# Optimization experiments

Hardware: AMD Instinct MI355X
Metric: run time of the kernel (lower is better)

Reference implementation:

```python
import jax, jax.numpy as jnp
import numpy as np

TOP_K = 2          # routed top_k = top_k - num_shared_experts = 3 - 1
CAP_FACTOR = 1.1   # capacity_factor


def setup_inputs() -> dict:
    key = jax.random.key(0)
    ks = jax.random.split(key, 12)
    B, S, D, E = 4, 2048, 1024, 7
    s = 0.02
    return {
        "x": jax.random.normal(ks[0], (B, S, D), jnp.float32),
        "noise": jax.random.normal(ks[1], (B, S, E), jnp.float32),
        "Wr": jax.random.normal(ks[2], (D, E)) * s, "br": jnp.zeros((E,)),
        "Wn": jax.random.normal(ks[3], (D, E)) * s, "bn": jnp.zeros((E,)),
        "W1": jax.random.normal(ks[4], (E, D, D)) * s, "b1": jnp.zeros((E, D)),
        "W2": jax.random.normal(ks[5], (E, D, D)) * s, "b2": jnp.zeros((E, D)),
        "Ws1": jax.random.normal(ks[6], (D, D)) * s, "bs1": jnp.zeros((D,)),
        "Ws2": jax.random.normal(ks[7], (D, D)) * s, "bs2": jnp.zeros((D,)),
    }


def reference(x, noise, Wr, br, Wn, bn, W1, b1, W2, b2, Ws1, bs1, Ws2, bs2):
    B, S, D = x.shape
    E = Wr.shape[1]
    N = B * S
    C = int(N * TOP_K / E * CAP_FACTOR)  # per-expert capacity (static)

    # shared expert (Dropout inactive at inference)
    x_shared = jax.nn.relu(x @ Ws1 + bs1) @ Ws2 + bs2

    # --- noisy top-k router ---
    logits = x @ Wr + br
    noisy = logits + noise * jax.nn.softplus(x @ Wn + bn)
    vals, idx = jax.lax.top_k(noisy, TOP_K)                    # [B,S,K]
    onehot = jax.nn.one_hot(idx, E, dtype=x.dtype)             # [B,S,K,E]
    probs_k = jax.nn.softmax(vals, axis=-1)                    # softmax over -inf-masked logits == softmax over top-k vals
    router_probs = jnp.einsum('bske,bsk->bse', onehot, probs_k)
    expert_mask = onehot.sum(-2)
    lbl = E * (router_probs.mean((0, 1)) * expert_mask.mean((0, 1))).sum()

    # --- capacity-limited dispatch, first-come-first-served in flat token order ---
    flat_x = x.reshape(N, D)
    flat_g = router_probs.reshape(N, E)
    m = (expert_mask.reshape(N, E) > 0).T                      # [E,N] token->expert assignment
    pos = jnp.cumsum(m.astype(jnp.int32), axis=1) - 1          # slot within expert
    valid = m & (pos < C)
    token = jnp.arange(N, dtype=jnp.int32)
    dest = jnp.where(valid, jnp.arange(E, dtype=jnp.int32)[:, None] * C + pos, E * C)
    idxs = jnp.full((E * C + 1,), N, dtype=jnp.int32)
    idxs = idxs.at[dest.reshape(-1)].set(jnp.broadcast_to(token, (E, N)).reshape(-1))
    idxs = idxs[:E * C].reshape(E, C)                          # token id per slot, N = padding

    xpad = jnp.concatenate([flat_x, jnp.zeros((1, D), x.dtype)], axis=0)
    gpad = jnp.concatenate([flat_g, jnp.zeros((1, E), x.dtype)], axis=0)
    xe = xpad[idxs]                                            # [E,C,D]
    h = jax.nn.relu(jnp.einsum('ecd,edh->ech', xe, W1) + b1[:, None, :])
    out = jnp.einsum('ech,ehd->ecd', h, W2) + b2[:, None, :]
    g = (gpad[idxs] * jnp.eye(E, dtype=x.dtype)[:, None, :]).sum(-1)  # [E,C] gate per slot
    slot_valid = (idxs < N).astype(x.dtype)
    weighted = out * (g * slot_valid)[..., None]

    upd = jnp.zeros((N + 1, D), x.dtype).at[idxs.reshape(-1)].add(weighted.reshape(-1, D))[:N]
    final = upd.reshape(B, S, D) + x_shared
    return final, lbl
```

## Files before the change

kernel.cpp:

```cpp
#include <hip/hip_runtime.h>
#include <math.h>

typedef unsigned short u16;
typedef __attribute__((ext_vector_type(4))) float f32x4;
typedef __bf16 bf16x8 __attribute__((ext_vector_type(8)));

#define NTOK 8192
#define DDIM 1024
#define NEXP 7
#define CAPC 2574
#define CPAD 2688
#define EBLK 1176
#define TBLK 1688

__device__ inline float bf2f(u16 u) {
    union { unsigned int i; float f; } c; c.i = ((unsigned int)u) << 16; return c.f;
}
__device__ inline u16 f2bf(float f) {
    union { float f; unsigned int i; } c; c.f = f;
    unsigned int u = c.i;
    unsigned int r = (u + 0x7fffu + ((u >> 16) & 1u)) >> 16;
    return (u16)r;
}

__device__ inline void gl2lds16(const u16* g, const u16* l) {
    __builtin_amdgcn_global_load_lds(
        (const __attribute__((address_space(1))) unsigned int*)g,
        (__attribute__((address_space(3))) unsigned int*)l, 16, 0, 0);
}

__global__ void k_zero(float* out, long n) {
    long i = (long)blockIdx.x * 256 + threadIdx.x;
    long stride = (long)gridDim.x * 256;
    for (; i < n; i += stride) out[i] = 0.f;
}

__global__ void k_prep(const float* __restrict__ x, u16* __restrict__ xb,
                       int* __restrict__ slot_token, u16* __restrict__ zrow,
                       const float* __restrict__ W1, const float* __restrict__ Ws1,
                       u16* __restrict__ Wt, u16* __restrict__ Wst,
                       const float* __restrict__ W2, const float* __restrict__ Ws2,
                       u16* __restrict__ Wt2, u16* __restrict__ Wst2) {
    int bid = blockIdx.x, tid = threadIdx.x;
    if (bid < 4096) {
        int gid = bid * 256 + tid;
        int i = gid * 8;
        float4 a = *(const float4*)(x + i);
        float4 b = *(const float4*)(x + i + 4);
        ushort4 o0; o0.x = f2bf(a.x); o0.y = f2bf(a.y); o0.z = f2bf(a.z); o0.w = f2bf(a.w);
        ushort4 o1; o1.x = f2bf(b.x); o1.y = f2bf(b.y); o1.z = f2bf(b.z); o1.w = f2bf(b.w);
        *(ushort4*)(xb + i) = o0;
        *(ushort4*)(xb + i + 4) = o1;
        if (gid < DDIM) zrow[gid] = 0;
        if (gid < NEXP * CPAD) slot_token[gid] = NTOK;
        return;
    }
    int phase2 = (bid >= 8192);
    int tb = bid - (phase2 ? 8192 : 4096);
    const float* srcE = phase2 ? W2 : W1;
    const float* srcS = phase2 ? Ws2 : Ws1;
    u16* dE = phase2 ? Wt2 : Wt;
    u16* dS = phase2 ? Wst2 : Wst;
    int z = tb >> 9; int rem = tb & 511;
    int y = rem >> 2; int xq = rem & 3;
    const float* src; u16* dst;
    if (z < 7) { src = srcE + (long)z * 1048576; dst = dE + (long)z * 1048576; }
    else       { src = srcS;                     dst = dS; }
    int n = xq * 256 + tid;
    int k0 = y * 8;
    u16 v[8];
#pragma unroll
    for (int j = 0; j < 8; ++j) v[j] = f2bf(src[(long)(k0 + j) * 1024 + n]);
    ushort4 a; a.x = v[0]; a.y = v[1]; a.z = v[2]; a.w = v[3];
    ushort4 b; b.x = v[4]; b.y = v[5]; b.z = v[6]; b.w = v[7];
    *(ushort4*)(dst + (long)n * 1024 + k0) = a;
    *(ushort4*)(dst + (long)n * 1024 + k0 + 4) = b;
}

__global__ void k_transpose(const float* __restrict__ srcE, const float* __restrict__ srcS,
                            u16* __restrict__ Wt, u16* __restrict__ Wst) {
    int z = blockIdx.z;
    const float* src; u16* dst;
    if (z < 7) { src = srcE + (long)z * 1048576; dst = Wt + (long)z * 1048576; }
    else       { src = srcS;                     dst = Wst; }
    int n = blockIdx.x * 256 + threadIdx.x;
    int k0 = blockIdx.y * 8;
    u16 v[8];
#pragma unroll
    for (int j = 0; j < 8; ++j) v[j] = f2bf(src[(long)(k0 + j) * 1024 + n]);
    ushort4 a; a.x = v[0]; a.y = v[1]; a.z = v[2]; a.w = v[3];
    ushort4 b; b.x = v[4]; b.y = v[5]; b.z = v[6]; b.w = v[7];
    *(ushort4*)(dst + (long)n * 1024 + k0) = a;
    *(ushort4*)(dst + (long)n * 1024 + k0 + 4) = b;
}

__global__ __launch_bounds__(512) void k_router(
    const float* __restrict__ x,
    const float* __restrict__ Wr, const float* __restrict__ Wn,
    double* __restrict__ arO, double* __restrict__ anO) {
    __shared__ float swr[7168];
    __shared__ float swn[7168];
    int tid = threadIdx.x;
    for (int i = tid; i < 7168; i += 512) { swr[i] = Wr[i]; swn[i] = Wn[i]; }
    __syncthreads();
    int lane = tid & 63, wv = tid >> 6;
    int t = blockIdx.x * 8 + wv;
    double ar[7] = {0,0,0,0,0,0,0}, an[7] = {0,0,0,0,0,0,0};
    for (int j = 0; j < 16; ++j) {
        int d = j * 64 + lane;
        double xd = (double)x[t * 1024 + d];
#pragma unroll
        for (int e = 0; e < 7; ++e) {
            ar[e] += xd * (double)swr[d * 7 + e];
            an[e] += xd * (double)swn[d * 7 + e];
        }
    }
#pragma unroll
    for (int e = 0; e < 7; ++e) {
        for (int o = 32; o > 0; o >>= 1) {
            ar[e] += __shfl_xor(ar[e], o);
            an[e] += __shfl_xor(an[e], o);
        }
    }
    if (lane == 0) {
#pragma unroll
        for (int e = 0; e < 7; ++e) { arO[t * 7 + e] = ar[e]; anO[t * 7 + e] = an[e]; }
    }
}

__global__ void k_tail(const double* __restrict__ arO, const double* __restrict__ anO,
                       const float* __restrict__ noise,
                       const float* __restrict__ br, const float* __restrict__ bn,
                       int* __restrict__ idx0, int* __restrict__ idx1,
                       float* __restrict__ p0, float* __restrict__ p1,
                       int* __restrict__ cntA, double* __restrict__ sumA) {
    int t = blockIdx.x * 256 + threadIdx.x;
    int lane = threadIdx.x & 63;
    double best = -1e300, second = -1e300; int b0 = 0, b1 = 0;
#pragma unroll
    for (int e = 0; e < 7; ++e) {
        double lg = arO[t * 7 + e] + (double)br[e];
        double z  = anO[t * 7 + e] + (double)bn[e];
        double sp = (z > 30.0) ? (z + log1p(exp(-z))) : log1p(exp(z));
        double v  = lg + (double)noise[t * 7 + e] * sp;
        if (v > best)        { second = best; b1 = b0; best = v; b0 = e; }
        else if (v > second) { second = v; b1 = e; }
    }
    double ex = exp(second - best);
    float q0 = (float)(1.0 / (1.0 + ex));
    float q1 = (float)(ex / (1.0 + ex));
    idx0[t] = b0; idx1[t] = b1; p0[t] = q0; p1[t] = q1;
    int chunk = t >> 6;
    double dq0 = (double)q0, dq1 = (double)q1;
#pragma unroll
    for (int e = 0; e < 7; ++e) {
        unsigned long long m = __ballot((b0 == e) || (b1 == e));
        double q = (b0 == e ? dq0 : 0.0) + (b1 == e ? dq1 : 0.0);
        for (int o = 32; o > 0; o >>= 1) q += __shfl_xor(q, o);
        if (lane == 0) { cntA[e * 128 + chunk] = __popcll(m); sumA[e * 128 + chunk] = q; }
    }
}

__global__ void k_scanbase(const int* __restrict__ cntA, const double* __restrict__ sumA,
                           int* __restrict__ baseA, int* __restrict__ cnt,
                           float* __restrict__ out) {
    __shared__ int s[128];
    __shared__ double rd[128];
    __shared__ int rawc[7];
    __shared__ double ps[7];
    int tid = threadIdx.x;
    for (int e = 0; e < 7; ++e) {
        int v = 0;
        if (tid < 128) { v = cntA[e * 128 + tid]; s[tid] = v; }
        if (tid < 128) rd[tid] = sumA[e * 128 + tid];
        __syncthreads();
        for (int o = 1; o < 128; o <<= 1) {
            int add = 0;
            if (tid < 128 && tid >= o) add = s[tid - o];
            __syncthreads();
            if (tid < 128) s[tid] += add;
            __syncthreads();
        }
        if (tid < 128) baseA[e * 128 + tid] = s[tid] - v;
        if (tid == 127) { rawc[e] = s[127]; cnt[e] = (s[127] < CAPC) ? s[127] : CAPC; }
        for (int o = 64; o > 0; o >>= 1) {
            if (tid < o) rd[tid] += rd[tid + o];
            __syncthreads();
        }
        if (tid == 0) ps[e] = rd[0];
        __syncthreads();
    }
    if (tid == 0) {
        double acc = 0.0;
        for (int e = 0; e < 7; ++e) acc += ps[e] * (double)rawc[e];
        out[(long)NTOK * DDIM] = (float)(7.0 * acc / (8192.0 * 8192.0));
    }
}

__global__ void k_assign(const int* __restrict__ idx0, const int* __restrict__ idx1,
                         const int* __restrict__ baseA, int* __restrict__ slot_token,
                         int* __restrict__ ts0, int* __restrict__ ts1) {
    int lane = threadIdx.x & 63;
    int chunk = (blockIdx.x * 256 + threadIdx.x) >> 6;
    int t = chunk * 64 + lane;
    int i0 = idx0[t], i1 = idx1[t];
    int myts0 = -1, myts1 = -1;
    unsigned long long lt = (1ull << lane) - 1ull;
#pragma unroll
    for (int e = 0; e < 7; ++e) {
        bool has = (i0 == e) || (i1 == e);
        unsigned long long m = __ballot(has);
        int pre = __popcll(m & lt);
        int pos = baseA[e * 128 + chunk] + pre;
        if (has && pos < CAPC) {
            int slot = e * CPAD + pos;
            slot_token[slot] = t;
            if (i0 == e) myts0 = slot; else myts1 = slot;
        }
    }
    ts0[t] = myts0; ts1[t] = myts1;
}

template <bool GATHER, bool MODE_H>
__global__ __launch_bounds__(256) void k_gemm(
    const u16* __restrict__ AbaseE, const u16* __restrict__ AbaseS,
    const int* __restrict__ gidx, const u16* __restrict__ zrow,
    const u16* __restrict__ WtE, const u16* __restrict__ WtS,
    const float* __restrict__ biasE, const float* __restrict__ biasS,
    u16* __restrict__ outE, u16* __restrict__ outS,
    const int* __restrict__ cnt) {
    __shared__ __align__(16) u16 ldsA[128 * 64];
    __shared__ __align__(16) u16 ldsB[128 * 64];
    int bid = blockIdx.x;
    int tid = threadIdx.x, lane = tid & 63, wv = tid >> 6;
    int lrow = lane >> 3, lkg = lane & 7;
    int kgs = lkg ^ lrow;

    int e = 0, my, nx;
    const u16* Ab; const u16* Bb; const float* bias; u16* outp;
    bool gather = false;
    if (bid < EBLK) {
        e = bid / 168; int r = bid % 168; my = r >> 3; nx = r & 7;
        if (my * 128 >= cnt[e]) return;
        Ab = AbaseE + (GATHER ? 0L : (long)e * CPAD * 1024);
        Bb = WtE + ((long)e << 20);
        bias = biasE + e * 1024;
        outp = outE + (long)e * CPAD * 1024;
        gather = GATHER;
    } else {
        int sb = bid - EBLK; my = sb >> 3; nx = sb & 7;
        Ab = AbaseS; Bb = WtS; bias = biasS; outp = outS;
    }
    int m0 = my * 128, n0 = nx * 128;

    const u16* arow[4];
    const u16* brow[4];
#pragma unroll
    for (int i = 0; i < 4; ++i) {
        int r = (wv * 4 + i) * 8 + lrow;
        if (gather) {
            int tok = gidx[e * CPAD + m0 + r];
            arow[i] = (tok < NTOK) ? (AbaseE + (long)tok * DDIM) : zrow;
        } else {
            arow[i] = Ab + (long)(m0 + r) * DDIM;
        }
        brow[i] = Bb + (long)(n0 + r) * DDIM;
    }
    f32x4 acc[4][4];
#pragma unroll
    for (int a = 0; a < 4; ++a)
#pragma unroll
        for (int b = 0; b < 4; ++b) { f32x4 z = {0.f, 0.f, 0.f, 0.f}; acc[a][b] = z; }

    int wm = (wv >> 1) * 64, wn = (wv & 1) * 64;
    int rl = lane & 15, quad = lane >> 4;

    for (int k0 = 0; k0 < 1024; k0 += 64) {
#pragma unroll
        for (int i = 0; i < 4; ++i) {
            gl2lds16(arow[i] + k0 + kgs * 8, &ldsA[(wv * 4 + i) * 512]);
            gl2lds16(brow[i] + k0 + kgs * 8, &ldsB[(wv * 4 + i) * 512]);
        }
        __syncthreads();
#pragma unroll
        for (int ks = 0; ks < 2; ++ks) {
            int kg = ks * 4 + quad;
            bf16x8 af[4], bf[4];
#pragma unroll
            for (int mi = 0; mi < 4; ++mi) {
                int row = wm + mi * 16 + rl;
                af[mi] = *(const bf16x8*)&ldsA[row * 64 + (kg ^ (row & 7)) * 8];
            }
#pragma unroll
            for (int ni = 0; ni < 4; ++ni) {
                int row = wn + ni * 16 + rl;
                bf[ni] = *(const bf16x8*)&ldsB[row * 64 + (kg ^ (row & 7)) * 8];
            }
#pragma unroll
            for (int mi = 0; mi < 4; ++mi)
#pragma unroll
                for (int ni = 0; ni < 4; ++ni)
                    acc[mi][ni] = __builtin_amdgcn_mfma_f32_16x16x32_bf16(
                        af[mi], bf[ni], acc[mi][ni], 0, 0, 0);
        }
        __syncthreads();
    }
#pragma unroll
    for (int ni = 0; ni < 4; ++ni) {
        int col = n0 + wn + ni * 16 + rl;
        float bv = bias[col];
#pragma unroll
        for (int mi = 0; mi < 4; ++mi) {
            int rowb = m0 + wm + mi * 16 + quad * 4;
#pragma unroll
            for (int r = 0; r < 4; ++r) {
                float v = acc[mi][ni][r] + bv;
                if constexpr (MODE_H) v = v > 0.f ? v : 0.f;
                outp[(long)(rowb + r) * DDIM + col] = f2bf(v);
            }
        }
    }
}

__global__ __launch_bounds__(256) void k_combine(
    const u16* __restrict__ Xs, const u16* __restrict__ OutE,
    const int* __restrict__ ts0, const int* __restrict__ ts1,
    const float* __restrict__ p0, const float* __restrict__ p1,
    float* __restrict__ out) {
    int b = blockIdx.x;
    int d = threadIdx.x * 4;
    long base = (long)b * DDIM + d;
    ushort4 xs4 = *(const ushort4*)(Xs + base);
    float r0 = bf2f(xs4.x), r1 = bf2f(xs4.y), r2 = bf2f(xs4.z), r3 = bf2f(xs4.w);
    int s0 = ts0[b], s1 = ts1[b];
    if (s0 >= 0) {
        float g = p0[b];
        ushort4 o4 = *(const ushort4*)(OutE + (long)s0 * DDIM + d);
        r0 += g * bf2f(o4.x); r1 += g * bf2f(o4.y); r2 += g * bf2f(o4.z); r3 += g * bf2f(o4.w);
    }
    if (s1 >= 0) {
        float g = p1[b];
        ushort4 o4 = *(const ushort4*)(OutE + (long)s1 * DDIM + d);
        r0 += g * bf2f(o4.x); r1 += g * bf2f(o4.y); r2 += g * bf2f(o4.z); r3 += g * bf2f(o4.w);
    }
    float4 w; w.x = r0; w.y = r1; w.z = r2; w.w = r3;
    *(float4*)(out + base) = w;
}

extern "C" void kernel_launch(void* const* d_in, const int* in_sizes, int n_in,
                              void* d_out, int out_size, void* d_ws, size_t ws_size,
                              hipStream_t stream) {
    const float* x    = (const float*)d_in[0];
    const float* noise= (const float*)d_in[1];
    const float* Wr   = (const float*)d_in[2];
    const float* br   = (const float*)d_in[3];
    const float* Wn   = (const float*)d_in[4];
    const float* bn   = (const float*)d_in[5];
    const float* W1   = (const float*)d_in[6];
    const float* b1   = (const float*)d_in[7];
    const float* W2   = (const float*)d_in[8];
    const float* b2   = (const float*)d_in[9];
    const float* Ws1  = (const float*)d_in[10];
    const float* bs1  = (const float*)d_in[11];
    const float* Ws2  = (const float*)d_in[12];
    const float* bs2  = (const float*)d_in[13];
    float* out = (float*)d_out;
    char* ws = (char*)d_ws;

    size_t off = 0;
    auto alloc = [&](size_t bytes) { size_t o = off; off += (bytes + 255) & ~(size_t)255; return o; };
    u16*  Wt   = (u16*)(ws + alloc(7ull * 1048576 * 2));
    u16*  Wst  = (u16*)(ws + alloc(1048576ull * 2));
    u16*  xb   = (u16*)(ws + alloc((size_t)NTOK * 1024 * 2));
    u16*  He   = (u16*)(ws + alloc((size_t)NEXP * CPAD * 1024 * 2));
    u16*  Hs   = (u16*)(ws + alloc((size_t)NTOK * 1024 * 2));
    u16*  OutE = (u16*)(ws + alloc((size_t)NEXP * CPAD * 1024 * 2));
    u16*  Xs   = (u16*)(ws + alloc((size_t)NTOK * 1024 * 2));
    int*  idx0 = (int*)(ws + alloc(NTOK * 4));
    int*  idx1 = (int*)(ws + alloc(NTOK * 4));
    float* p0  = (float*)(ws + alloc(NTOK * 4));
    float* p1  = (float*)(ws + alloc(NTOK * 4));
    int*  ts0  = (int*)(ws + alloc(NTOK * 4));
    int*  ts1  = (int*)(ws + alloc(NTOK * 4));
    int*  slot_token = (int*)(ws + alloc(NEXP * CPAD * 4));
    int*  cntA = (int*)(ws + alloc(7 * 128 * 4));
    int*  baseA= (int*)(ws + alloc(7 * 128 * 4));
    double* sumA = (double*)(ws + alloc(7 * 128 * 8));
    int*  cnt    = (int*)(ws + alloc(8 * 4));
    u16*  zrow   = (u16*)(ws + alloc(1024 * 2));
    double* arO  = (double*)(ws + alloc((size_t)NTOK * 7 * 8));
    double* anO  = (double*)(ws + alloc((size_t)NTOK * 7 * 8));
    size_t base_off = off;
    u16*  Wt2  = (u16*)(ws + alloc(7ull * 1048576 * 2));
    u16*  Wst2 = (u16*)(ws + alloc(1048576ull * 2));

    if (base_off > ws_size) {
        k_zero<<<2048, 256, 0, stream>>>(out, (long)out_size);
        return;
    }
    bool sep = (off <= ws_size);
    if (!sep) { Wt2 = Wt; Wst2 = Wst; }

    k_prep<<<sep ? 12288 : 8192, 256, 0, stream>>>(
        x, xb, slot_token, zrow, W1, Ws1, Wt, Wst, W2, Ws2, Wt2, Wst2);
    k_router<<<1024, 512, 0, stream>>>(x, Wr, Wn, arO, anO);
    k_tail<<<32, 256, 0, stream>>>(arO, anO, noise, br, bn, idx0, idx1, p0, p1, cntA, sumA);
    k_scanbase<<<1, 256, 0, stream>>>(cntA, sumA, baseA, cnt, out);
    k_assign<<<32, 256, 0, stream>>>(idx0, idx1, baseA, slot_token, ts0, ts1);

    k_gemm<true, true><<<TBLK, 256, 0, stream>>>(
        xb, xb, slot_token, zrow, Wt, Wst, b1, bs1, He, Hs, cnt);

    if (!sep)
        k_transpose<<<dim3(4, 128, 8), 256, 0, stream>>>(W2, Ws2, Wt, Wst);

    k_gemm<false, false><<<TBLK, 256, 0, stream>>>(
        He, Hs, nullptr, zrow, Wt2, Wst2, b2, bs2, OutE, Xs, cnt);

    k_combine<<<NTOK, 256, 0, stream>>>(Xs, OutE, ts0, ts1, p0, p1, out);
    (void)in_sizes; (void)n_in; (void)out_size;
}
```

Measured before the change: 401.1 us.

## Double-buffer GEMM LDS with inline-asm reads, tile weight transpose via LDS, parallelize scan

```diff
diff --git a/kernel.cpp b/kernel.cpp
--- a/kernel.cpp
+++ b/kernel.cpp
@@ -3,6 +3,7 @@
 
 typedef unsigned short u16;
 typedef __attribute__((ext_vector_type(4))) float f32x4;
+typedef __attribute__((ext_vector_type(4))) int v4i;
 typedef __bf16 bf16x8 __attribute__((ext_vector_type(8)));
 
 #define NTOK 8192
@@ -29,10 +30,45 @@
         (__attribute__((address_space(3))) unsigned int*)l, 16, 0, 0);
 }
 
+#define SCHED0()  __builtin_amdgcn_sched_barrier(0)
+#define PRIO1()   __builtin_amdgcn_s_setprio(1)
+#define PRIO0()   __builtin_amdgcn_s_setprio(0)
+#define LGKM8()   asm volatile("s_waitcnt lgkmcnt(8)")
+#define LGKM0()   asm volatile("s_waitcnt lgkmcnt(0)")
+
 __global__ void k_zero(float* out, long n) {
     long i = (long)blockIdx.x * 256 + threadIdx.x;
     long stride = (long)gridDim.x * 256;
     for (; i < n; i += stride) out[i] = 0.f;
+}
+
+__device__ inline void tile_transpose(const float* __restrict__ src, u16* __restrict__ dst,
+                                      int k0, int n0, int tid, u16 (*tbuf)[256]) {
+#pragma unroll
+    for (int p = 0; p < 16; ++p) {
+        int kl = p * 16 + (tid >> 4);
+        int nl = (tid & 15) * 4;
+        float4 v = *(const float4*)(src + (long)(k0 + kl) * 1024 + n0 + nl);
+        int s = (tid & 7) << 3;
+        int kx = kl ^ s;
+        tbuf[nl + 0][kx] = f2bf(v.x);
+        tbuf[nl + 1][kx] = f2bf(v.y);
+        tbuf[nl + 2][kx] = f2bf(v.z);
+        tbuf[nl + 3][kx] = f2bf(v.w);
+    }
+    __syncthreads();
+#pragma unroll
+    for (int q = 0; q < 8; ++q) {
+        int nl = q * 8 + (tid >> 5);
+        int kl = (tid & 31) * 8;
+        int s = ((nl >> 2) & 7) << 3;
+        const u16* pr = &tbuf[nl][kl ^ s];
+        ushort4 a = *(const ushort4*)pr;
+        ushort4 b = *(const ushort4*)(pr + 4);
+        u16* pd = dst + (long)(n0 + nl) * 1024 + k0 + kl;
+        *(ushort4*)pd = a;
+        *(ushort4*)(pd + 4) = b;
+    }
 }
 
 __global__ void k_prep(const float* __restrict__ x, u16* __restrict__ xb,
@@ -41,6 +77,7 @@
                        u16* __restrict__ Wt, u16* __restrict__ Wst,
                        const float* __restrict__ W2, const float* __restrict__ Ws2,
                        u16* __restrict__ Wt2, u16* __restrict__ Wst2) {
+    __shared__ u16 tbuf[64][256];
     int bid = blockIdx.x, tid = threadIdx.x;
     if (bid < 4096) {
         int gid = bid * 256 + tid;
@@ -55,43 +92,35 @@
         if (gid < NEXP * CPAD) slot_token[gid] = NTOK;
         return;
     }
-    int phase2 = (bid >= 8192);
-    int tb = bid - (phase2 ? 8192 : 4096);
-    const float* srcE = phase2 ? W2 : W1;
-    const float* srcS = phase2 ? Ws2 : Ws1;
-    u16* dE = phase2 ? Wt2 : Wt;
-    u16* dS = phase2 ? Wst2 : Wst;
-    int z = tb >> 9; int rem = tb & 511;
-    int y = rem >> 2; int xq = rem & 3;
+    int tb = bid - 4096;
+    int set = tb >> 9;
+    int t9 = tb & 511;
+    int z = t9 >> 6;
+    int rem = t9 & 63;
+    int k0 = (rem >> 4) * 256;
+    int n0 = (rem & 15) * 64;
+    const float* srcE = set ? W2 : W1;
+    const float* srcS = set ? Ws2 : Ws1;
+    u16* dE = set ? Wt2 : Wt;
+    u16* dS = set ? Wst2 : Wst;
     const float* src; u16* dst;
     if (z < 7) { src = srcE + (long)z * 1048576; dst = dE + (long)z * 1048576; }
     else       { src = srcS;                     dst = dS; }
-    int n = xq * 256 + tid;
-    int k0 = y * 8;
-    u16 v[8];
-#pragma unroll
-    for (int j = 0; j < 8; ++j) v[j] = f2bf(src[(long)(k0 + j) * 1024 + n]);
-    ushort4 a; a.x = v[0]; a.y = v[1]; a.z = v[2]; a.w = v[3];
-    ushort4 b; b.x = v[4]; b.y = v[5]; b.z = v[6]; b.w = v[7];
-    *(ushort4*)(dst + (long)n * 1024 + k0) = a;
-    *(ushort4*)(dst + (long)n * 1024 + k0 + 4) = b;
+    tile_transpose(src, dst, k0, n0, tid, tbuf);
 }
 
 __global__ void k_transpose(const float* __restrict__ srcE, const float* __restrict__ srcS,
                             u16* __restrict__ Wt, u16* __restrict__ Wst) {
-    int z = blockIdx.z;
+    __shared__ u16 tbuf[64][256];
+    int bid = blockIdx.x, tid = threadIdx.x;
+    int z = bid >> 6;
+    int rem = bid & 63;
+    int k0 = (rem >> 4) * 256;
+    int n0 = (rem & 15) * 64;
     const float* src; u16* dst;
     if (z < 7) { src = srcE + (long)z * 1048576; dst = Wt + (long)z * 1048576; }
     else       { src = srcS;                     dst = Wst; }
-    int n = blockIdx.x * 256 + threadIdx.x;
-    int k0 = blockIdx.y * 8;
-    u16 v[8];
-#pragma unroll
-    for (int j = 0; j < 8; ++j) v[j] = f2bf(src[(long)(k0 + j) * 1024 + n]);
-    ushort4 a; a.x = v[0]; a.y = v[1]; a.z = v[2]; a.w = v[3];
-    ushort4 b; b.x = v[4]; b.y = v[5]; b.z = v[6]; b.w = v[7];
-    *(ushort4*)(dst + (long)n * 1024 + k0) = a;
-    *(ushort4*)(dst + (long)n * 1024 + k0 + 4) = b;
+    tile_transpose(src, dst, k0, n0, tid, tbuf);
 }
 
 __global__ __launch_bounds__(512) void k_router(
@@ -164,35 +193,33 @@
 __global__ void k_scanbase(const int* __restrict__ cntA, const double* __restrict__ sumA,
                            int* __restrict__ baseA, int* __restrict__ cnt,
                            float* __restrict__ out) {
-    __shared__ int s[128];
-    __shared__ double rd[128];
+    __shared__ int s[7][128];
+    __shared__ double rd[7][128];
     __shared__ int rawc[7];
     __shared__ double ps[7];
     int tid = threadIdx.x;
-    for (int e = 0; e < 7; ++e) {
-        int v = 0;
-        if (tid < 128) { v = cntA[e * 128 + tid]; s[tid] = v; }
-        if (tid < 128) rd[tid] = sumA[e * 128 + tid];
+    int e = tid >> 7, i = tid & 127;
+    int v = cntA[e * 128 + i];
+    s[e][i] = v;
+    rd[e][i] = sumA[e * 128 + i];
+    __syncthreads();
+    for (int o = 1; o < 128; o <<= 1) {
+        int add = (i >= o) ? s[e][i - o] : 0;
         __syncthreads();
-        for (int o = 1; o < 128; o <<= 1) {
-            int add = 0;
-            if (tid < 128 && tid >= o) add = s[tid - o];
-            __syncthreads();
-            if (tid < 128) s[tid] += add;
-            __syncthreads();
-        }
-        if (tid < 128) baseA[e * 128 + tid] = s[tid] - v;
-        if (tid == 127) { rawc[e] = s[127]; cnt[e] = (s[127] < CAPC) ? s[127] : CAPC; }
-        for (int o = 64; o > 0; o >>= 1) {
-            if (tid < o) rd[tid] += rd[tid + o];
-            __syncthreads();
-        }
-        if (tid == 0) ps[e] = rd[0];
+        s[e][i] += add;
         __syncthreads();
     }
+    baseA[e * 128 + i] = s[e][i] - v;
+    if (i == 127) { rawc[e] = s[e][127]; cnt[e] = (s[e][127] < CAPC) ? s[e][127] : CAPC; }
+    for (int o = 64; o > 0; o >>= 1) {
+        if (i < o) rd[e][i] += rd[e][i + o];
+        __syncthreads();
+    }
+    if (i == 0) ps[e] = rd[e][0];
+    __syncthreads();
     if (tid == 0) {
         double acc = 0.0;
-        for (int e = 0; e < 7; ++e) acc += ps[e] * (double)rawc[e];
+        for (int ee = 0; ee < 7; ++ee) acc += ps[ee] * (double)rawc[ee];
         out[(long)NTOK * DDIM] = (float)(7.0 * acc / (8192.0 * 8192.0));
     }
 }
@@ -221,6 +248,37 @@
     ts0[t] = myts0; ts1[t] = myts1;
 }
 
+
+union Fr { v4i i; bf16x8 h; };
+
+#define DSR(DST, ADDR, OFF) \
+    asm volatile("ds_read_b128 %0, %1 offset:%c2" : "=v"(DST) : "v"(ADDR), "i"(OFF));
+
+#define RDQ(BUF)                                              \
+    _Pragma("unroll")                                         \
+    for (int mi = 0; mi < 4; ++mi) { DSR(af0[mi].i, aA0, (BUF) * 16384 + mi * 2048) } \
+    _Pragma("unroll")                                         \
+    for (int ni = 0; ni < 4; ++ni) { DSR(bf0[ni].i, aB0, (BUF) * 16384 + ni * 2048) } \
+    _Pragma("unroll")                                         \
+    for (int mi = 0; mi < 4; ++mi) { DSR(af1[mi].i, aA1, (BUF) * 16384 + mi * 2048) } \
+    _Pragma("unroll")                                         \
+    for (int ni = 0; ni < 4; ++ni) { DSR(bf1[ni].i, aB1, (BUF) * 16384 + ni * 2048) }
+
+#define MFMAS(AF, BF)                                         \
+    _Pragma("unroll")                                         \
+    for (int mi = 0; mi < 4; ++mi)                            \
+        _Pragma("unroll")                                     \
+        for (int ni = 0; ni < 4; ++ni)                        \
+            acc[mi][ni] = __builtin_amdgcn_mfma_f32_16x16x32_bf16( \
+                AF[mi].h, BF[ni].h, acc[mi][ni], 0, 0, 0);
+
+#define STG(BUF, K)                                           \
+    _Pragma("unroll")                                         \
+    for (int i = 0; i < 4; ++i) {                             \
+        gl2lds16(arow[i] + (K) + kgs * 8, &ldsA[BUF][(wv * 4 + i) * 512]); \
+        gl2lds16(brow[i] + (K) + kgs * 8, &ldsB[BUF][(wv * 4 + i) * 512]); \
+    }
+
 template <bool GATHER, bool MODE_H>
 __global__ __launch_bounds__(256) void k_gemm(
     const u16* __restrict__ AbaseE, const u16* __restrict__ AbaseS,
@@ -229,8 +287,8 @@
     const float* __restrict__ biasE, const float* __restrict__ biasS,
     u16* __restrict__ outE, u16* __restrict__ outS,
     const int* __restrict__ cnt) {
-    __shared__ __align__(16) u16 ldsA[128 * 64];
-    __shared__ __align__(16) u16 ldsB[128 * 64];
+    __shared__ __align__(16) u16 ldsA[2][8192];
+    __shared__ __align__(16) u16 ldsB[2][8192];
     int bid = blockIdx.x;
     int tid = threadIdx.x, lane = tid & 63, wv = tid >> 6;
     int lrow = lane >> 3, lkg = lane & 7;
@@ -273,38 +331,41 @@
         for (int b = 0; b < 4; ++b) { f32x4 z = {0.f, 0.f, 0.f, 0.f}; acc[a][b] = z; }
 
     int wm = (wv >> 1) * 64, wn = (wv & 1) * 64;
-    int rl = lane & 15, quad = lane >> 4;
-
-    for (int k0 = 0; k0 < 1024; k0 += 64) {
-#pragma unroll
-        for (int i = 0; i < 4; ++i) {
-            gl2lds16(arow[i] + k0 + kgs * 8, &ldsA[(wv * 4 + i) * 512]);
-            gl2lds16(brow[i] + k0 + kgs * 8, &ldsB[(wv * 4 + i) * 512]);
-        }
+    int rl = lane & 15, quad = lane >> 4, kq7 = rl & 7;
+
+    unsigned bA = (unsigned)(uintptr_t)(__attribute__((address_space(3))) u16*)&ldsA[0][0];
+    unsigned bB = (unsigned)(uintptr_t)(__attribute__((address_space(3))) u16*)&ldsB[0][0];
+    int sw0 = ((quad ^ kq7) & 7) * 16;
+    int aA0 = (int)bA + (wm + rl) * 128 + sw0;
+    int aA1 = aA0 ^ 64;
+    int aB0 = (int)bB + (wn + rl) * 128 + sw0;
+    int aB1 = aB0 ^ 64;
+
+    Fr af0[4], af1[4], bf0[4], bf1[4];
+
+    STG(0, 0)
+    __syncthreads();
+
+    for (int tt = 0; tt < 8; ++tt) {
+        int kc = tt * 128;
+        STG(1, kc + 64)
+        RDQ(0)
+        LGKM8(); SCHED0();
+        PRIO1(); MFMAS(af0, bf0) PRIO0();
+        LGKM0(); SCHED0();
+        PRIO1(); MFMAS(af1, bf1) PRIO0();
         __syncthreads();
-#pragma unroll
-        for (int ks = 0; ks < 2; ++ks) {
-            int kg = ks * 4 + quad;
-            bf16x8 af[4], bf[4];
-#pragma unroll
-            for (int mi = 0; mi < 4; ++mi) {
-                int row = wm + mi * 16 + rl;
-                af[mi] = *(const bf16x8*)&ldsA[row * 64 + (kg ^ (row & 7)) * 8];
-            }
-#pragma unroll
-            for (int ni = 0; ni < 4; ++ni) {
-                int row = wn + ni * 16 + rl;
-                bf[ni] = *(const bf16x8*)&ldsB[row * 64 + (kg ^ (row & 7)) * 8];
-            }
-#pragma unroll
-            for (int mi = 0; mi < 4; ++mi)
-#pragma unroll
-                for (int ni = 0; ni < 4; ++ni)
-                    acc[mi][ni] = __builtin_amdgcn_mfma_f32_16x16x32_bf16(
-                        af[mi], bf[ni], acc[mi][ni], 0, 0, 0);
-        }
+        if (tt < 7) {
+            STG(0, kc + 128)
+        }
+        RDQ(1)
+        LGKM8(); SCHED0();
+        PRIO1(); MFMAS(af0, bf0) PRIO0();
+        LGKM0(); SCHED0();
+        PRIO1(); MFMAS(af1, bf1) PRIO0();
         __syncthreads();
     }
+
 #pragma unroll
     for (int ni = 0; ni < 4; ++ni) {
         int col = n0 + wn + ni * 16 + rl;
@@ -401,18 +462,18 @@
     bool sep = (off <= ws_size);
     if (!sep) { Wt2 = Wt; Wst2 = Wst; }
 
-    k_prep<<<sep ? 12288 : 8192, 256, 0, stream>>>(
+    k_prep<<<sep ? 5120 : 4608, 256, 0, stream>>>(
         x, xb, slot_token, zrow, W1, Ws1, Wt, Wst, W2, Ws2, Wt2, Wst2);
     k_router<<<1024, 512, 0, stream>>>(x, Wr, Wn, arO, anO);
     k_tail<<<32, 256, 0, stream>>>(arO, anO, noise, br, bn, idx0, idx1, p0, p1, cntA, sumA);
-    k_scanbase<<<1, 256, 0, stream>>>(cntA, sumA, baseA, cnt, out);
+    k_scanbase<<<1, 896, 0, stream>>>(cntA, sumA, baseA, cnt, out);
     k_assign<<<32, 256, 0, stream>>>(idx0, idx1, baseA, slot_token, ts0, ts1);
 
     k_gemm<true, true><<<TBLK, 256, 0, stream>>>(
         xb, xb, slot_token, zrow, Wt, Wst, b1, bs1, He, Hs, cnt);
 
     if (!sep)
-        k_transpose<<<dim3(4, 128, 8), 256, 0, stream>>>(W2, Ws2, Wt, Wst);
+        k_transpose<<<512, 256, 0, stream>>>(W2, Ws2, Wt, Wst);
 
     k_gemm<false, false><<<TBLK, 256, 0, stream>>>(
         He, Hs, nullptr, zrow, Wt2, Wst2, b2, bs2, OutE, Xs, cnt);
```

After: 415.3 us. 1.04x slower.
